# Kernel optimization log

Measured on AMD Instinct MI355X. Metric: run time of the kernel, lower is better.

The kernel has to match this reference:

```python
import jax, jax.numpy as jnp
import numpy as np


def setup_inputs() -> dict:
    key = jax.random.key(0)
    k1, k2 = jax.random.split(key)
    N, C, K = 65536, 128, 1024  # N = batch*emb_sample_len flattened latents
    z_e = jax.random.normal(k1, (N, C), dtype=jnp.float32)
    # nn.Embedding codebook; original inits uniform(-1/K, 1/K), randn is fine for a numeric reference
    codebook = jax.random.normal(k2, (K, C), dtype=jnp.float32) * 0.02
    return {"z_e": z_e, "codebook": codebook}


def reference(z_e, codebook):
    """VQ-VAE quantizer core: cdist + argmin nearest-codebook lookup,
    commitment loss (0.75 * q_latent + e_latent), straight-through estimator.
    z_e: [N, C] flattened encoder latents; codebook: [K, C].
    """
    # Squared euclidean distances, expanded form (same argmin as torch.cdist)
    ze_sq = jnp.sum(z_e * z_e, axis=1, keepdims=True)          # [N, 1]
    cb_sq = jnp.sum(codebook * codebook, axis=1)                # [K]
    cross = jnp.einsum('nc,kc->nk', z_e, codebook)              # [N, K]
    dist_sq = ze_sq - 2.0 * cross + cb_sq[None, :]              # [N, K]
    encoding_indices = jnp.argmin(dist_sq, axis=1)              # [N] int

    z_q = codebook[encoding_indices]                            # [N, C] gather

    # commitment loss: 0.75 * mse(stop_grad(z_e), z_q) + mse(z_e, stop_grad(z_q))
    q_latent_loss = jnp.mean((jax.lax.stop_gradient(z_e) - z_q) ** 2)
    e_latent_loss = jnp.mean((z_e - jax.lax.stop_gradient(z_q)) ** 2)
    commitment_loss = 0.75 * q_latent_loss + e_latent_loss

    # straight-through estimator (training path)
    z_q_st = z_e + jax.lax.stop_gradient(z_q - z_e)
    return z_q_st, commitment_loss, encoding_indices
```

## Files before the change

### kernel.cpp

```cpp
#include <hip/hip_runtime.h>

#define N_TOT 65536
#define C_DIM 128
#define K_CB  1024
#define BN 64
#define BT 64
#define NTILE (K_CB / BT)
#define ROWS_BLK 8
#define NBLK_R (N_TOT / ROWS_BLK)

typedef __attribute__((ext_vector_type(8))) short bf16x8;
typedef __attribute__((ext_vector_type(4))) float f32x4;

__device__ __forceinline__ ushort f2bf_rne(float f) {
  unsigned u = __float_as_uint(f);
  return (ushort)((u + 0x7FFFu + ((u >> 16) & 1u)) >> 16);
}

__device__ __forceinline__ unsigned med3u(unsigned a, unsigned b, unsigned c) {
  unsigned d;
  asm("v_med3_u32 %0, %1, %2, %3" : "=v"(d) : "v"(a), "v"(b), "v"(c));
  return d;
}

#define GLDS16(src, dst)                                                       \
  __builtin_amdgcn_global_load_lds(                                            \
      (const __attribute__((address_space(1))) void*)(src),                    \
      (__attribute__((address_space(3))) void*)(dst), 16, 0, 0)

__global__ __launch_bounds__(256) void prep_kernel(
    const float* __restrict__ cb, float* __restrict__ cbsq,
    ushort* __restrict__ cbh) {
  int w = threadIdx.x >> 6, lane = threadIdx.x & 63;
  int r = blockIdx.x * 4 + w;
  float2 v = reinterpret_cast<const float2*>(cb + (size_t)r * C_DIM)[lane];
  ushort2 h;
  h.x = f2bf_rne(v.x); h.y = f2bf_rne(v.y);
  reinterpret_cast<ushort2*>(cbh + (size_t)r * C_DIM)[lane] = h;
  double s = (double)v.x * (double)v.x + (double)v.y * (double)v.y;
#pragma unroll
  for (int off = 32; off >= 1; off >>= 1) s += __shfl_xor(s, off, 64);
  if (lane == 0) cbsq[r] = (float)s;
}

__global__ __launch_bounds__(256, 4) void dist_mfma_kernel(
    const float* __restrict__ ze, const ushort* __restrict__ cbh,
    const float* __restrict__ cbsq, ushort* __restrict__ cand) {
  __shared__ __align__(16) char smem[36864];
  char* const B0 = smem;
  char* const B1 = smem + 16384;
  ushort* zhS = reinterpret_cast<ushort*>(B1);
  unsigned* pool = reinterpret_cast<unsigned*>(smem);
  float* const cbsqS = reinterpret_cast<float*>(smem + 32768);

  const int tid = threadIdx.x;
  const int w = tid >> 6, lane = tid & 63;
  const int mh = w & 1, nh = w >> 1;
  const int c16 = lane & 15, quad = lane >> 4;
  const int rowbase = blockIdx.x * BN;

  int soff[4];
#pragma unroll
  for (int i = 0; i < 4; ++i) {
    int o = w * 4096 + i * 1024 + lane * 16;
    int row = o >> 8, inrow = o & 255;
    soff[i] = row * 256 + (inrow ^ ((row & 7) << 4));
  }
  const int stoff = w * 4096;

#pragma unroll
  for (int i = 0; i < 4; ++i)
    GLDS16((const char*)cbh + soff[i], B0 + stoff + i * 1024);

#pragma unroll
  for (int p = 0; p < 4; ++p) {
    int fid = p * 256 + tid;
    int row = fid >> 4, c8 = fid & 15;
    float4 a = reinterpret_cast<const float4*>(ze)[(size_t)(rowbase + row) * 32 + c8 * 2];
    float4 b = reinterpret_cast<const float4*>(ze)[(size_t)(rowbase + row) * 32 + c8 * 2 + 1];
    ushort h[8] = {f2bf_rne(a.x), f2bf_rne(a.y), f2bf_rne(a.z), f2bf_rne(a.w),
                   f2bf_rne(b.x), f2bf_rne(b.y), f2bf_rne(b.z), f2bf_rne(b.w)};
    *reinterpret_cast<uint4*>(&zhS[row * 128 + ((c8 ^ (row & 7)) * 8)]) =
        *reinterpret_cast<const uint4*>(h);
  }
  reinterpret_cast<float4*>(cbsqS)[tid] = reinterpret_cast<const float4*>(cbsq)[tid];
  __syncthreads();

  const int xk = c16 & 7;
  bf16x8 afrag[2][4];
#pragma unroll
  for (int m2 = 0; m2 < 2; ++m2) {
    int r = (mh * 32 + m2 * 16 + c16) * 128;
#pragma unroll
    for (int ks = 0; ks < 4; ++ks)
      afrag[m2][ks] = *reinterpret_cast<const bf16x8*>(&zhS[r + ((ks * 4 + quad) ^ xk) * 8]);
  }
  __syncthreads();

  unsigned t3[8][3];
#pragma unroll
  for (int s = 0; s < 8; ++s) { t3[s][0] = 0xFFFFFFFFu; t3[s][1] = 0xFFFFFFFFu; t3[s][2] = 0xFFFFFFFFu; }

  const int cbase = nh * 32 + c16;

  auto STAGE = [&](int t, char* dst) {
#pragma unroll
    for (int i = 0; i < 4; ++i)
      GLDS16((const char*)cbh + (size_t)t * 16384 + soff[i], dst + stoff + i * 1024);
  };
  auto READ_MFMA = [&](const char* buf, f32x4 (&acc)[2][2]) {
    bf16x8 bf[2][4];
#pragma unroll
    for (int n2 = 0; n2 < 2; ++n2) {
      int rb = (nh * 32 + n2 * 16 + c16) * 256;
#pragma unroll
      for (int ks = 0; ks < 4; ++ks)
        bf[n2][ks] = *reinterpret_cast<const bf16x8*>(buf + rb + (((ks * 4 + quad) ^ xk) << 4));
    }
#pragma unroll
    for (int m2 = 0; m2 < 2; ++m2)
#pragma unroll
      for (int n2 = 0; n2 < 2; ++n2) acc[m2][n2] = (f32x4){0.f, 0.f, 0.f, 0.f};
#pragma unroll
    for (int ks = 0; ks < 4; ++ks)
#pragma unroll
      for (int m2 = 0; m2 < 2; ++m2)
#pragma unroll
        for (int n2 = 0; n2 < 2; ++n2)
          acc[m2][n2] = __builtin_amdgcn_mfma_f32_16x16x32_bf16(afrag[m2][ks], bf[n2][ks], acc[m2][n2], 0, 0, 0);
  };
  auto SORT = [&](const f32x4 (&acc)[2][2], int t) {
#pragma unroll
    for (int n2 = 0; n2 < 2; ++n2) {
      int code = t * BT + cbase + n2 * 16;
      unsigned codeu = (unsigned)code & 1023u;
      float csb = cbsqS[code] + 192.0f;
#pragma unroll
      for (int m2 = 0; m2 < 2; ++m2)
#pragma unroll
        for (int reg = 0; reg < 4; ++reg) {
          float kf = fmaf(-2.f, acc[m2][n2][reg], csb);
          unsigned pk = (__float_as_uint(kf) & 0xFFFFFC00u) | codeu;
          int s = m2 * 4 + reg;
          unsigned n0 = min(t3[s][0], pk);
          unsigned n1 = med3u(t3[s][0], t3[s][1], pk);
          unsigned n2v = med3u(t3[s][1], t3[s][2], pk);
          t3[s][0] = n0; t3[s][1] = n1; t3[s][2] = n2v;
        }
    }
  };

  f32x4 accA[2][2], accB[2][2];

  STAGE(1, B1);
  READ_MFMA(B0, accA);
  __syncthreads();

  for (int tp = 0; tp < 7; ++tp) {
    int t = 2 * tp + 1;
    STAGE(t + 1, B0);
    SORT(accA, t - 1);
    READ_MFMA(B1, accB);
    __syncthreads();
    STAGE(t + 2, B1);
    SORT(accB, t);
    READ_MFMA(B0, accA);
    __syncthreads();
  }
  SORT(accA, 14);
  READ_MFMA(B1, accB);
  SORT(accB, 15);
  __syncthreads();

#pragma unroll
  for (int s = 0; s < 8; ++s) {
    int row = mh * 32 + (s >> 2) * 16 + quad * 4 + (s & 3);
    int col = (nh * 16 + c16) * 3;
    pool[row * 97 + col] = t3[s][0];
    pool[row * 97 + col + 1] = t3[s][1];
    pool[row * 97 + col + 2] = t3[s][2];
  }
  __syncthreads();
  if (tid < BN) {
    unsigned k[8];
#pragma unroll
    for (int q = 0; q < 8; ++q) k[q] = 0xFFFFFFFFu;
    for (int p = 0; p < 96; ++p) {
      unsigned v = pool[tid * 97 + p];
      if (v < k[7]) {
        k[7] = v;
#pragma unroll
        for (int q = 7; q > 0; --q)
          if (k[q] < k[q - 1]) { unsigned tk = k[q]; k[q] = k[q - 1]; k[q - 1] = tk; }
      }
    }
    uint4 cw;
    cw.x = (k[0] & 1023u) | ((k[1] & 1023u) << 16);
    cw.y = (k[2] & 1023u) | ((k[3] & 1023u) << 16);
    cw.z = (k[4] & 1023u) | ((k[5] & 1023u) << 16);
    cw.w = (k[6] & 1023u) | ((k[7] & 1023u) << 16);
    reinterpret_cast<uint4*>(cand)[rowbase + tid] = cw;
  }
}

__global__ __launch_bounds__(256) void rescore_kernel(
    const float* __restrict__ ze, const float* __restrict__ cb,
    const float* __restrict__ cbsq, const ushort* __restrict__ cand,
    float* __restrict__ zq, float* __restrict__ idx_f,
    double* __restrict__ partial) {
  int w = threadIdx.x >> 6, lane = threadIdx.x & 63;
  int h = lane >> 5, sl = lane & 31;
  int row = blockIdx.x * ROWS_BLK + w * 2 + h;
  int g = sl >> 2, e = sl & 3;
  int myc = cand[(size_t)row * 8 + g];

  const float4* zr = reinterpret_cast<const float4*>(ze + (size_t)row * C_DIM);
  const float4* cr = reinterpret_cast<const float4*>(cb + (size_t)myc * C_DIM);

  double p0 = 0.0, p1 = 0.0, zs0 = 0.0, zs1 = 0.0;
#pragma unroll
  for (int j = 0; j < 8; ++j) {
    float4 zf = zr[e + 4 * j];
    float4 cf = cr[e + 4 * j];
    double a = ((double)zf.x * (double)cf.x + (double)zf.y * (double)cf.y) +
               ((double)zf.z * (double)cf.z + (double)zf.w * (double)cf.w);
    double b = ((double)zf.x * (double)zf.x + (double)zf.y * (double)zf.y) +
               ((double)zf.z * (double)zf.z + (double)zf.w * (double)zf.w);
    if (j & 1) { p1 += a; zs1 += b; } else { p0 += a; zs0 += b; }
  }
  double pp = p0 + p1;
  double zsum = zs0 + zs1;
  pp += __shfl_xor(pp, 1, 64);
  pp += __shfl_xor(pp, 2, 64);
  zsum += __shfl_xor(zsum, 1, 64);
  zsum += __shfl_xor(zsum, 2, 64);

  float zs = (float)zsum;
  float tt = (float)(2.0 * pp);
  float u = zs - tt;
  float d = u + cbsq[myc];

#pragma unroll
  for (int off = 4; off <= 16; off <<= 1) {
    float dg = __shfl_xor(d, off, 64);
    int ig = __shfl_xor(myc, off, 64);
    if (dg < d || (dg == d && ig < myc)) { d = dg; myc = ig; }
  }

  const float4* cbest = reinterpret_cast<const float4*>(cb + (size_t)myc * C_DIM);
  float4 cl = cbest[sl];
  float4 zl = zr[sl];
  reinterpret_cast<float4*>(zq + (size_t)row * C_DIM)[sl] = cl;

  double dx = (double)zl.x - (double)cl.x;
  double dy = (double)zl.y - (double)cl.y;
  double dz = (double)zl.z - (double)cl.z;
  double dw = (double)zl.w - (double)cl.w;
  double l = (dx * dx + dy * dy) + (dz * dz + dw * dw);
#pragma unroll
  for (int off = 1; off <= 32; off <<= 1) l += __shfl_xor(l, off, 64);

  if (sl == 0) idx_f[row] = (float)myc;
  __shared__ double sh[4];
  if (lane == 0) sh[w] = l;
  __syncthreads();
  if (threadIdx.x == 0)
    partial[blockIdx.x] = (sh[0] + sh[1]) + (sh[2] + sh[3]);
}

__global__ __launch_bounds__(256) void finalize_kernel(
    const double* __restrict__ partial, float* __restrict__ out_loss) {
  double s = 0.0;
  for (int i = threadIdx.x; i < NBLK_R; i += 256) s += partial[i];
#pragma unroll
  for (int off = 32; off >= 1; off >>= 1) s += __shfl_down(s, off, 64);
  __shared__ double sh[4];
  int wv = threadIdx.x >> 6, lane = threadIdx.x & 63;
  if (lane == 0) sh[wv] = s;
  __syncthreads();
  if (threadIdx.x == 0) {
    double tot = sh[0] + sh[1] + sh[2] + sh[3];
    double mse = tot / (double)((size_t)N_TOT * C_DIM);
    *out_loss = (float)(1.75 * mse);
  }
}

extern "C" void kernel_launch(void* const* d_in, const int* in_sizes, int n_in,
                              void* d_out, int out_size, void* d_ws, size_t ws_size,
                              hipStream_t stream) {
  const float* ze = (const float*)d_in[0];
  const float* cb = (const float*)d_in[1];

  float* out = (float*)d_out;
  float* zq = out;
  float* out_loss = out + (size_t)N_TOT * C_DIM;
  float* idx_f = out_loss + 1;

  float* cbsq = (float*)d_ws;
  ushort* cbh = (ushort*)((char*)d_ws + 8192);
  ushort* cand = (ushort*)((char*)d_ws + 270336);
  double* partial = (double*)((char*)d_ws + 1318912);

  prep_kernel<<<K_CB / 4, 256, 0, stream>>>(cb, cbsq, cbh);
  dist_mfma_kernel<<<N_TOT / BN, 256, 0, stream>>>(ze, cbh, cbsq, cand);
  rescore_kernel<<<NBLK_R, 256, 0, stream>>>(ze, cb, cbsq, cand, zq, idx_f, partial);
  finalize_kernel<<<1, 256, 0, stream>>>(partial, out_loss);
}
```

Measured before the change: 151.3 us.

## Fuse fp64 rescore stage into the MFMA distance kernel via shared-memory candidates

Merges the rescore kernel into the bf16 MFMA distance kernel. Each block keeps its top-8 candidate list in shared memory and loops over its 64 rows to rescore them exactly, write z_q and the indices, and accumulate the loss partial. This removes one kernel launch and the global round trip for the candidate array, and the z_e rows may still be cache-resident when they are reread. In exchange the rescore runs serially inside the distance kernel with fewer blocks, so latency hiding may suffer. The candidate buffer also aliases shared memory used by the pool and by cbsq.

```diff
diff --git a/kernel.cpp b/kernel.cpp
--- a/kernel.cpp
+++ b/kernel.cpp
@@ -6,8 +6,7 @@
 #define BN 64
 #define BT 64
 #define NTILE (K_CB / BT)
-#define ROWS_BLK 8
-#define NBLK_R (N_TOT / ROWS_BLK)
+#define NBLK_D (N_TOT / BN)
 
 typedef __attribute__((ext_vector_type(8))) short bf16x8;
 typedef __attribute__((ext_vector_type(4))) float f32x4;
@@ -43,15 +42,19 @@
   if (lane == 0) cbsq[r] = (float)s;
 }
 
-__global__ __launch_bounds__(256, 4) void dist_mfma_kernel(
+__global__ __launch_bounds__(256, 4) void dist_rescore_kernel(
     const float* __restrict__ ze, const ushort* __restrict__ cbh,
-    const float* __restrict__ cbsq, ushort* __restrict__ cand) {
+    const float* __restrict__ cbsq, const float* __restrict__ cb,
+    float* __restrict__ zq, float* __restrict__ idx_f,
+    double* __restrict__ partial) {
   __shared__ __align__(16) char smem[36864];
   char* const B0 = smem;
   char* const B1 = smem + 16384;
   ushort* zhS = reinterpret_cast<ushort*>(B1);
   unsigned* pool = reinterpret_cast<unsigned*>(smem);
   float* const cbsqS = reinterpret_cast<float*>(smem + 32768);
+  ushort* const candS = reinterpret_cast<ushort*>(smem + 30720);
+  double* const shl = reinterpret_cast<double*>(smem + 32768);
 
   const int tid = threadIdx.x;
   const int w = tid >> 6, lane = tid & 63;
@@ -199,79 +202,79 @@
     cw.y = (k[2] & 1023u) | ((k[3] & 1023u) << 16);
     cw.z = (k[4] & 1023u) | ((k[5] & 1023u) << 16);
     cw.w = (k[6] & 1023u) | ((k[7] & 1023u) << 16);
-    reinterpret_cast<uint4*>(cand)[rowbase + tid] = cw;
-  }
-}
-
-__global__ __launch_bounds__(256) void rescore_kernel(
-    const float* __restrict__ ze, const float* __restrict__ cb,
-    const float* __restrict__ cbsq, const ushort* __restrict__ cand,
-    float* __restrict__ zq, float* __restrict__ idx_f,
-    double* __restrict__ partial) {
-  int w = threadIdx.x >> 6, lane = threadIdx.x & 63;
-  int h = lane >> 5, sl = lane & 31;
-  int row = blockIdx.x * ROWS_BLK + w * 2 + h;
-  int g = sl >> 2, e = sl & 3;
-  int myc = cand[(size_t)row * 8 + g];
-
-  const float4* zr = reinterpret_cast<const float4*>(ze + (size_t)row * C_DIM);
-  const float4* cr = reinterpret_cast<const float4*>(cb + (size_t)myc * C_DIM);
-
-  double p0 = 0.0, p1 = 0.0, zs0 = 0.0, zs1 = 0.0;
-#pragma unroll
-  for (int j = 0; j < 8; ++j) {
-    float4 zf = zr[e + 4 * j];
-    float4 cf = cr[e + 4 * j];
-    double a = ((double)zf.x * (double)cf.x + (double)zf.y * (double)cf.y) +
-               ((double)zf.z * (double)cf.z + (double)zf.w * (double)cf.w);
-    double b = ((double)zf.x * (double)zf.x + (double)zf.y * (double)zf.y) +
-               ((double)zf.z * (double)zf.z + (double)zf.w * (double)zf.w);
-    if (j & 1) { p1 += a; zs1 += b; } else { p0 += a; zs0 += b; }
-  }
-  double pp = p0 + p1;
-  double zsum = zs0 + zs1;
-  pp += __shfl_xor(pp, 1, 64);
-  pp += __shfl_xor(pp, 2, 64);
-  zsum += __shfl_xor(zsum, 1, 64);
-  zsum += __shfl_xor(zsum, 2, 64);
-
-  float zs = (float)zsum;
-  float tt = (float)(2.0 * pp);
-  float u = zs - tt;
-  float d = u + cbsq[myc];
-
-#pragma unroll
-  for (int off = 4; off <= 16; off <<= 1) {
-    float dg = __shfl_xor(d, off, 64);
-    int ig = __shfl_xor(myc, off, 64);
-    if (dg < d || (dg == d && ig < myc)) { d = dg; myc = ig; }
-  }
-
-  const float4* cbest = reinterpret_cast<const float4*>(cb + (size_t)myc * C_DIM);
-  float4 cl = cbest[sl];
-  float4 zl = zr[sl];
-  reinterpret_cast<float4*>(zq + (size_t)row * C_DIM)[sl] = cl;
-
-  double dx = (double)zl.x - (double)cl.x;
-  double dy = (double)zl.y - (double)cl.y;
-  double dz = (double)zl.z - (double)cl.z;
-  double dw = (double)zl.w - (double)cl.w;
-  double l = (dx * dx + dy * dy) + (dz * dz + dw * dw);
-#pragma unroll
-  for (int off = 1; off <= 32; off <<= 1) l += __shfl_xor(l, off, 64);
-
-  if (sl == 0) idx_f[row] = (float)myc;
-  __shared__ double sh[4];
-  if (lane == 0) sh[w] = l;
-  __syncthreads();
-  if (threadIdx.x == 0)
-    partial[blockIdx.x] = (sh[0] + sh[1]) + (sh[2] + sh[3]);
+    reinterpret_cast<uint4*>(candS)[tid] = cw;
+  }
+  __syncthreads();
+
+  const int h2 = lane >> 5, sl = lane & 31;
+  const int g = sl >> 2, e = sl & 3;
+  double lacc = 0.0;
+#pragma unroll 1
+  for (int it = 0; it < 8; ++it) {
+    int rl = it * 8 + w * 2 + h2;
+    int row = rowbase + rl;
+    int myc = candS[rl * 8 + g];
+
+    const float4* zr = reinterpret_cast<const float4*>(ze + (size_t)row * C_DIM);
+    const float4* cr = reinterpret_cast<const float4*>(cb + (size_t)myc * C_DIM);
+
+    double p0 = 0.0, p1 = 0.0, zs0 = 0.0, zs1 = 0.0;
+#pragma unroll
+    for (int j = 0; j < 8; ++j) {
+      float4 zf = zr[e + 4 * j];
+      float4 cf = cr[e + 4 * j];
+      double a = ((double)zf.x * (double)cf.x + (double)zf.y * (double)cf.y) +
+                 ((double)zf.z * (double)cf.z + (double)zf.w * (double)cf.w);
+      double b = ((double)zf.x * (double)zf.x + (double)zf.y * (double)zf.y) +
+                 ((double)zf.z * (double)zf.z + (double)zf.w * (double)zf.w);
+      if (j & 1) { p1 += a; zs1 += b; } else { p0 += a; zs0 += b; }
+    }
+    double pp = p0 + p1;
+    double zsum = zs0 + zs1;
+    pp += __shfl_xor(pp, 1, 64);
+    pp += __shfl_xor(pp, 2, 64);
+    zsum += __shfl_xor(zsum, 1, 64);
+    zsum += __shfl_xor(zsum, 2, 64);
+
+    float zs = (float)zsum;
+    float tt = (float)(2.0 * pp);
+    float u = zs - tt;
+    float d = u + cbsq[myc];
+
+#pragma unroll
+    for (int off = 4; off <= 16; off <<= 1) {
+      float dg = __shfl_xor(d, off, 64);
+      int ig = __shfl_xor(myc, off, 64);
+      if (dg < d || (dg == d && ig < myc)) { d = dg; myc = ig; }
+    }
+
+    const float4* cbest = reinterpret_cast<const float4*>(cb + (size_t)myc * C_DIM);
+    float4 cl = cbest[sl];
+    float4 zl = zr[sl];
+    reinterpret_cast<float4*>(zq + (size_t)row * C_DIM)[sl] = cl;
+
+    double dx = (double)zl.x - (double)cl.x;
+    double dy = (double)zl.y - (double)cl.y;
+    double dz = (double)zl.z - (double)cl.z;
+    double dw = (double)zl.w - (double)cl.w;
+    double l = (dx * dx + dy * dy) + (dz * dz + dw * dw);
+#pragma unroll
+    for (int off = 1; off <= 32; off <<= 1) l += __shfl_xor(l, off, 64);
+    lacc += l;
+
+    if (sl == 0) idx_f[row] = (float)myc;
+  }
+
+  if (lane == 0) shl[w] = lacc;
+  __syncthreads();
+  if (tid == 0)
+    partial[blockIdx.x] = (shl[0] + shl[1]) + (shl[2] + shl[3]);
 }
 
 __global__ __launch_bounds__(256) void finalize_kernel(
     const double* __restrict__ partial, float* __restrict__ out_loss) {
   double s = 0.0;
-  for (int i = threadIdx.x; i < NBLK_R; i += 256) s += partial[i];
+  for (int i = threadIdx.x; i < NBLK_D; i += 256) s += partial[i];
 #pragma unroll
   for (int off = 32; off >= 1; off >>= 1) s += __shfl_down(s, off, 64);
   __shared__ double sh[4];
@@ -298,11 +301,10 @@
 
   float* cbsq = (float*)d_ws;
   ushort* cbh = (ushort*)((char*)d_ws + 8192);
-  ushort* cand = (ushort*)((char*)d_ws + 270336);
-  double* partial = (double*)((char*)d_ws + 1318912);
+  double* partial = (double*)((char*)d_ws + 270336);
 
   prep_kernel<<<K_CB / 4, 256, 0, stream>>>(cb, cbsq, cbh);
-  dist_mfma_kernel<<<N_TOT / BN, 256, 0, stream>>>(ze, cbh, cbsq, cand);
-  rescore_kernel<<<NBLK_R, 256, 0, stream>>>(ze, cb, cbsq, cand, zq, idx_f, partial);
+  dist_rescore_kernel<<<NBLK_D, 256, 0, stream>>>(ze, cbh, cbsq, cb, zq,
+                                                  idx_f, partial);
   finalize_kernel<<<1, 256, 0, stream>>>(partial, out_loss);
 }
```

Result: faster. 135.2 us (-10.7%).
